# Kernel optimization log

Measured on AMD Instinct MI355X. Metric: run time of the kernel, lower is better.

## Reference

```python
import jax, jax.numpy as jnp
import numpy as np

L, D, C, H = 2, 2, 256, 128  # layers, directions, channels, hidden (= C//2, bidirectional)
B, T = 32, 1024


def setup_inputs() -> dict:
    key = jax.random.key(0)
    ks = jax.random.split(key, 5)
    k = 1.0 / np.sqrt(H)  # PyTorch LSTM init scale
    u = lambda kk, shape: jax.random.uniform(kk, shape, jnp.float32, -k, k)
    return {
        "x": jax.random.normal(ks[0], (B, C, T), jnp.float32),
        "W_ih": u(ks[1], (L, D, 4 * H, C)),  # layer1 input is concat(fwd,bwd) = C wide too
        "W_hh": u(ks[2], (L, D, 4 * H, H)),
        "b_ih": u(ks[3], (L, D, 4 * H)),
        "b_hh": u(ks[4], (L, D, 4 * H)),
    }


def _lstm_dir(xs, Wih, Whh, bih, bhh, reverse):
    # xs: [T, B, C_in] time-major; returns hidden states [T, B, H]
    Tn, Bn, _ = xs.shape
    Hh = Whh.shape[1]
    # precompute input contribution to all gates for every timestep (one big GEMM)
    gx = jnp.einsum('tbc,gc->tbg', xs, Wih) + bih + bhh  # [T, B, 4H]

    def step(carry, g):
        h, c = carry
        g = g + h @ Whh.T  # [B, 4H]
        i, f, gg, o = jnp.split(g, 4, axis=-1)  # PyTorch gate order: i, f, g, o
        c = jax.nn.sigmoid(f) * c + jax.nn.sigmoid(i) * jnp.tanh(gg)
        h = jax.nn.sigmoid(o) * jnp.tanh(c)
        return (h, c), h

    init = (jnp.zeros((Bn, Hh), xs.dtype), jnp.zeros((Bn, Hh), xs.dtype))
    _, hs = jax.lax.scan(step, init, gx, reverse=reverse)
    return hs


def reference(x, W_ih, W_hh, b_ih, b_hh):
    # x: [B, C, T] -> time-major [T, B, C] (matches x.transpose(1,2) with batch_first)
    h = jnp.transpose(x, (2, 0, 1))
    for l in range(L):
        fwd = _lstm_dir(h, W_ih[l, 0], W_hh[l, 0], b_ih[l, 0], b_hh[l, 0], False)
        bwd = _lstm_dir(h, W_ih[l, 1], W_hh[l, 1], b_ih[l, 1], b_hh[l, 1], True)
        h = jnp.concatenate([fwd, bwd], axis=-1)  # [T, B, 2H] = [T, B, C]
    # back to [B, C, T] (matches out.transpose(1,2))
    return jnp.transpose(h, (1, 2, 0))
```

## Files before the change

kernel.cpp:

```cpp
#include <hip/hip_runtime.h>
#include <cstdint>
#include <cstddef>

static constexpr int TT = 1024;
static constexpr int BB = 32;
static constexpr int CC = 256;
static constexpr int HH = 128;
static constexpr int GG = 512;
static constexpr int MM = TT * BB;

typedef float f32x2 __attribute__((ext_vector_type(2)));
typedef float f32x4v __attribute__((ext_vector_type(4)));
typedef short bf16x8 __attribute__((ext_vector_type(8)));

__device__ __forceinline__ float fsig(float x) { return 1.f / (1.f + __expf(-x)); }
__device__ __forceinline__ float ftanh(float x) {
  float e = __expf(2.f * x);
  return 1.f - 2.f / (e + 1.f);
}
__device__ __forceinline__ ushort bf16_rn(float x) {
  union { float f; uint u; } v; v.f = x;
  const uint r = v.u + 0x7fffu + ((v.u >> 16) & 1u);
  return (ushort)(r >> 16);
}
__device__ __forceinline__ float bf16_to_f(ushort h) {
  union { uint u; float f; } v; v.u = ((uint)h) << 16;
  return v.f;
}
__device__ __forceinline__ uint pack2(ushort a, ushort b) { return (uint)a | ((uint)b << 16); }

__global__ __launch_bounds__(256) void k_transpose_cvt_in(const float* __restrict__ x,
                                                          ushort* __restrict__ xhi,
                                                          ushort* __restrict__ xlo) {
  __shared__ float tile[32][33];
  const int t0 = blockIdx.x * 32, c0 = blockIdx.y * 32, b = blockIdx.z;
  const int tx = threadIdx.x, ty = threadIdx.y;
#pragma unroll
  for (int i = 0; i < 4; i++) {
    const int cc = ty + i * 8;
    tile[cc][tx] = x[((size_t)b * CC + (c0 + cc)) * TT + t0 + tx];
  }
  __syncthreads();
#pragma unroll
  for (int i = 0; i < 4; i++) {
    const int tt = ty + i * 8;
    const float v = tile[tx][tt];
    const ushort hi = bf16_rn(v);
    const size_t idx = ((size_t)(t0 + tt) * BB + b) * CC + c0 + tx;
    xhi[idx] = hi;
    xlo[idx] = bf16_rn(v - bf16_to_f(hi));
  }
}

__global__ __launch_bounds__(256) void k_transpose_out(const float* __restrict__ h2,
                                                       float* __restrict__ out) {
  __shared__ float tile[32][33];
  const int t0 = blockIdx.x * 32, c0 = blockIdx.y * 32, b = blockIdx.z;
  const int tx = threadIdx.x, ty = threadIdx.y;
#pragma unroll
  for (int i = 0; i < 4; i++) {
    const int tt = ty + i * 8;
    tile[tt][tx] = h2[((size_t)(t0 + tt) * BB + b) * CC + c0 + tx];
  }
  __syncthreads();
#pragma unroll
  for (int i = 0; i < 4; i++) {
    const int cc = ty + i * 8;
    out[((size_t)b * CC + (c0 + cc)) * TT + t0 + tx] = tile[tx][cc];
  }
}

__global__ __launch_bounds__(256) void k_gemm_mfma(const ushort* __restrict__ Ahi,
                                                   const ushort* __restrict__ Alo,
                                                   const float* __restrict__ W,
                                                   const float* __restrict__ bih,
                                                   const float* __restrict__ bhh,
                                                   float* __restrict__ gx) {
  const int d = blockIdx.z;
  const int g0 = blockIdx.x * 64;
  const int m0 = blockIdx.y * 128;
  const float* Wd = W + (size_t)d * GG * CC;

  __shared__ ushort Ah[128][64];
  __shared__ ushort Al[128][64];
  __shared__ ushort Bh[64][64];
  __shared__ ushort Bl[64][64];

  const int tid = threadIdx.x;
  const int lane = tid & 63;
  const int wid = tid >> 6;
  const int wm = (wid >> 1) * 64;
  const int wg = (wid & 1) * 32;

  f32x4v acc[4][2] = {};

  for (int k0 = 0; k0 < CC; k0 += 64) {
    __syncthreads();
#pragma unroll
    for (int c = 0; c < 4; c++) {
      const int f8 = c * 256 + tid;
      const int r = f8 >> 3;
      const int kb = f8 & 7;
      const int sw = (kb ^ (r & 7)) << 3;
      const uint4 vh = *(const uint4*)&Ahi[(size_t)(m0 + r) * CC + k0 + kb * 8];
      const uint4 vl = *(const uint4*)&Alo[(size_t)(m0 + r) * CC + k0 + kb * 8];
      *(uint4*)&Ah[r][sw] = vh;
      *(uint4*)&Al[r][sw] = vl;
    }
#pragma unroll
    for (int c = 0; c < 4; c++) {
      const int f4 = c * 256 + tid;
      const int g = f4 >> 4;
      const int k4 = f4 & 15;
      const float4 wv = *(const float4*)&Wd[(size_t)(g0 + g) * CC + k0 + k4 * 4];
      ushort h0 = bf16_rn(wv.x), h1 = bf16_rn(wv.y), h2 = bf16_rn(wv.z), h3 = bf16_rn(wv.w);
      ushort l0 = bf16_rn(wv.x - bf16_to_f(h0)), l1 = bf16_rn(wv.y - bf16_to_f(h1));
      ushort l2 = bf16_rn(wv.z - bf16_to_f(h2)), l3 = bf16_rn(wv.w - bf16_to_f(h3));
      const int off = (((k4 >> 1) ^ (g & 7)) << 3) | ((k4 & 1) * 4);
      uint2 ph; ph.x = pack2(h0, h1); ph.y = pack2(h2, h3);
      uint2 pl; pl.x = pack2(l0, l1); pl.y = pack2(l2, l3);
      *(uint2*)&Bh[g][off] = ph;
      *(uint2*)&Bl[g][off] = pl;
    }
    __syncthreads();
#pragma unroll
    for (int h = 0; h < 2; h++) {
      const int kb = h * 4 + (lane >> 4);
      bf16x8 afh[4], afl[4], bfh[2], bfl[2];
#pragma unroll
      for (int i = 0; i < 4; i++) {
        const int row = wm + i * 16 + (lane & 15);
        const int sw = (kb ^ (row & 7)) << 3;
        afh[i] = *(const bf16x8*)&Ah[row][sw];
        afl[i] = *(const bf16x8*)&Al[row][sw];
      }
#pragma unroll
      for (int j = 0; j < 2; j++) {
        const int gr = wg + j * 16 + (lane & 15);
        const int sw = (kb ^ (gr & 7)) << 3;
        bfh[j] = *(const bf16x8*)&Bh[gr][sw];
        bfl[j] = *(const bf16x8*)&Bl[gr][sw];
      }
#pragma unroll
      for (int i = 0; i < 4; i++)
#pragma unroll
        for (int j = 0; j < 2; j++) {
          acc[i][j] = __builtin_amdgcn_mfma_f32_16x16x32_bf16(afh[i], bfh[j], acc[i][j], 0, 0, 0);
          acc[i][j] = __builtin_amdgcn_mfma_f32_16x16x32_bf16(afh[i], bfl[j], acc[i][j], 0, 0, 0);
          acc[i][j] = __builtin_amdgcn_mfma_f32_16x16x32_bf16(afl[i], bfh[j], acc[i][j], 0, 0, 0);
        }
    }
  }
  const int col = lane & 15;
  const int rbase = (lane >> 4) * 4;
#pragma unroll
  for (int j = 0; j < 2; j++) {
    const int g = g0 + wg + j * 16 + col;
    const float bias = bih[d * GG + g] + bhh[d * GG + g];
#pragma unroll
    for (int i = 0; i < 4; i++) {
      const int mrow = m0 + wm + i * 16 + rbase;
#pragma unroll
      for (int rr = 0; rr < 4; rr++)
        gx[((size_t)d * MM + mrow + rr) * GG + g] = acc[i][j][rr] + bias;
    }
  }
}

__global__ __launch_bounds__(512, 1) void k_lstm_rec(const float* __restrict__ gx,
                                                     const float* __restrict__ Whh,
                                                     float* __restrict__ hf32,
                                                     ushort* __restrict__ hhi,
                                                     ushort* __restrict__ hlo,
                                                     int store_bf16) {
  const int b = blockIdx.x & 31;
  const int d = blockIdx.x >> 5;
  const int tid = threadIdx.x;
  const int q = tid >> 7;
  const int j = tid & 127;
  __shared__ __align__(16) float h_s[HH];
  __shared__ __align__(16) float part[4][HH][4];

  f32x2 w2[4][16];
  {
    const float* base = Whh + (size_t)d * GG * HH;
#pragma unroll
    for (int gi = 0; gi < 4; gi++) {
      const float4* wrow = (const float4*)(base + (size_t)(gi * HH + j) * HH + q * 32);
#pragma unroll
      for (int k = 0; k < 8; k++) {
        const float4 t4 = wrow[k];
        w2[gi][2 * k] = f32x2{t4.x, t4.y};
        w2[gi][2 * k + 1] = f32x2{t4.z, t4.w};
      }
    }
  }
#pragma unroll
  for (int gi = 0; gi < 4; gi++)
#pragma unroll
    for (int k = 0; k < 16; k++)
      asm volatile("" : "+v"(w2[gi][k]));

  if (tid < HH) h_s[tid] = 0.f;
  float c = 0.f;

  const float* gxb = gx + ((size_t)d * TT * BB + b) * (size_t)GG;
  const size_t stride = (size_t)BB * GG;
  int t = d ? (TT - 1) : 0;
  const int tdir = d ? -1 : 1;
  const bool is_act = (tid < HH);

  float gxc0 = 0.f, gxc1 = 0.f, gxc2 = 0.f, gxc3 = 0.f;
  if (is_act) {
    const float* g0 = gxb + (size_t)t * stride + j;
    gxc0 = g0[0]; gxc1 = g0[HH]; gxc2 = g0[2 * HH]; gxc3 = g0[3 * HH];
  }
  __syncthreads();

  for (int s = 0; s < TT; s++) {
    float gxn0 = 0.f, gxn1 = 0.f, gxn2 = 0.f, gxn3 = 0.f;
    if (is_act && s + 1 < TT) {
      const float* g0 = gxb + (size_t)(t + tdir) * stride + j;
      gxn0 = g0[0]; gxn1 = g0[HH]; gxn2 = g0[2 * HH]; gxn3 = g0[3 * HH];
    }

    f32x2 hp[16];
    {
      const float4* hq = (const float4*)(h_s + q * 32);
#pragma unroll
      for (int k = 0; k < 8; k++) {
        const float4 hv = hq[k];
        hp[2 * k] = f32x2{hv.x, hv.y};
        hp[2 * k + 1] = f32x2{hv.z, hv.w};
      }
    }

    f32x2 aA0 = {0.f, 0.f}, aA1 = {0.f, 0.f}, aA2 = {0.f, 0.f}, aA3 = {0.f, 0.f};
    f32x2 aB0 = {0.f, 0.f}, aB1 = {0.f, 0.f}, aB2 = {0.f, 0.f}, aB3 = {0.f, 0.f};
#pragma unroll
    for (int k = 0; k < 8; k++) {
      aA0 = w2[0][2 * k] * hp[2 * k] + aA0;  aB0 = w2[0][2 * k + 1] * hp[2 * k + 1] + aB0;
      aA1 = w2[1][2 * k] * hp[2 * k] + aA1;  aB1 = w2[1][2 * k + 1] * hp[2 * k + 1] + aB1;
      aA2 = w2[2][2 * k] * hp[2 * k] + aA2;  aB2 = w2[2][2 * k + 1] * hp[2 * k + 1] + aB2;
      aA3 = w2[3][2 * k] * hp[2 * k] + aA3;  aB3 = w2[3][2 * k + 1] * hp[2 * k + 1] + aB3;
    }
    const float A0 = (aA0.x + aA0.y) + (aB0.x + aB0.y);
    const float A1 = (aA1.x + aA1.y) + (aB1.x + aB1.y);
    const float A2 = (aA2.x + aA2.y) + (aB2.x + aB2.y);
    const float A3 = (aA3.x + aA3.y) + (aB3.x + aB3.y);
    *(float4*)&part[q][j][0] = make_float4(A0, A1, A2, A3);
    __syncthreads();

    if (is_act) {
      const float4 p0 = *(const float4*)&part[0][j][0];
      const float4 p1 = *(const float4*)&part[1][j][0];
      const float4 p2 = *(const float4*)&part[2][j][0];
      const float4 p3 = *(const float4*)&part[3][j][0];
      const float i_g = fsig(p0.x + p1.x + p2.x + p3.x + gxc0);
      const float f_g = fsig(p0.y + p1.y + p2.y + p3.y + gxc1);
      const float g_g = ftanh(p0.z + p1.z + p2.z + p3.z + gxc2);
      const float o_g = fsig(p0.w + p1.w + p2.w + p3.w + gxc3);
      c = f_g * c + i_g * g_g;
      const float h = o_g * ftanh(c);
      h_s[j] = h;
      const size_t idx = ((size_t)t * BB + b) * CC + d * HH + j;
      if (store_bf16) {
        const ushort hi = bf16_rn(h);
        hhi[idx] = hi;
        hlo[idx] = bf16_rn(h - bf16_to_f(hi));
      } else {
        hf32[idx] = h;
      }
    }
    __syncthreads();
    gxc0 = gxn0; gxc1 = gxn1; gxc2 = gxn2; gxc3 = gxn3;
    t += tdir;
  }
}

extern "C" void kernel_launch(void* const* d_in, const int* in_sizes, int n_in,
                              void* d_out, int out_size, void* d_ws, size_t ws_size,
                              hipStream_t stream) {
  const float* x    = (const float*)d_in[0];
  const float* W_ih = (const float*)d_in[1];
  const float* W_hh = (const float*)d_in[2];
  const float* b_ih = (const float*)d_in[3];
  const float* b_hh = (const float*)d_in[4];
  float* out = (float*)d_out;

  if (ws_size < (size_t)160 * 1024 * 1024) return;

  char* ws = (char*)d_ws;
  ushort* abf_hi = (ushort*)ws;
  ushort* abf_lo = (ushort*)(ws + (size_t)16 * 1024 * 1024);
  float*  h2     = (float*)ws;
  float*  gxbuf  = (float*)(ws + (size_t)32 * 1024 * 1024);

  const dim3 tb(32, 8);
  const dim3 tg(TT / 32, CC / 32, BB);
  const dim3 gemm_grid(GG / 64, MM / 128, 2);

  k_transpose_cvt_in<<<tg, tb, 0, stream>>>(x, abf_hi, abf_lo);
  k_gemm_mfma<<<gemm_grid, 256, 0, stream>>>(abf_hi, abf_lo, W_ih, b_ih, b_hh, gxbuf);
  k_lstm_rec<<<64, 512, 0, stream>>>(gxbuf, W_hh, nullptr, abf_hi, abf_lo, 1);
  k_gemm_mfma<<<gemm_grid, 256, 0, stream>>>(abf_hi, abf_lo, W_ih + 2 * GG * CC,
                                             b_ih + 2 * GG, b_hh + 2 * GG, gxbuf);
  k_lstm_rec<<<64, 512, 0, stream>>>(gxbuf, W_hh + 2 * GG * HH, h2, nullptr, nullptr, 0);
  k_transpose_out<<<tg, tb, 0, stream>>>(h2, out);
}
```

Before: 1.819 ms.

## Reduce LSTM recurrence partials via lane shuffles and double-buffer hidden state

The recurrent kernel now places the four K-quarter partial sums of each hidden unit in adjacent lanes of one wavefront and combines them with xor-shuffles, replacing the shared-memory partial array and one of the two block barriers per timestep. The hidden state is double-buffered in LDS so a single barrier per step suffices. That barrier waits only on LDS counters, not on global stores. Every thread now runs the gate math redundantly, and the h outputs are written by different lanes to spread the stores. The intent is to cut per-step synchronisation latency on the serial time loop.

```diff
diff --git a/kernel.cpp b/kernel.cpp
--- a/kernel.cpp
+++ b/kernel.cpp
@@ -9,7 +9,6 @@
 static constexpr int GG = 512;
 static constexpr int MM = TT * BB;
 
-typedef float f32x2 __attribute__((ext_vector_type(2)));
 typedef float f32x4v __attribute__((ext_vector_type(4)));
 typedef short bf16x8 __attribute__((ext_vector_type(8)));
 
@@ -28,6 +27,12 @@
   return v.f;
 }
 __device__ __forceinline__ uint pack2(ushort a, ushort b) { return (uint)a | ((uint)b << 16); }
+
+__device__ __forceinline__ void barrier_lds_only() {
+  asm volatile("s_waitcnt lgkmcnt(0)" ::: "memory");
+  __builtin_amdgcn_s_barrier();
+  asm volatile("" ::: "memory");
+}
 
 __global__ __launch_bounds__(256) void k_transpose_cvt_in(const float* __restrict__ x,
                                                           ushort* __restrict__ xhi,
@@ -176,103 +181,92 @@
   const int b = blockIdx.x & 31;
   const int d = blockIdx.x >> 5;
   const int tid = threadIdx.x;
-  const int q = tid >> 7;
-  const int j = tid & 127;
-  __shared__ __align__(16) float h_s[HH];
-  __shared__ __align__(16) float part[4][HH][4];
-
-  f32x2 w2[4][16];
+  const int lane = tid & 63;
+  const int m = lane >> 2;
+  const int q = lane & 3;
+  const int j = (tid >> 6) * 16 + m;
+
+  __shared__ __align__(16) float h_s[2][HH];
+
+  float4 w4[4][8];
   {
     const float* base = Whh + (size_t)d * GG * HH;
 #pragma unroll
     for (int gi = 0; gi < 4; gi++) {
       const float4* wrow = (const float4*)(base + (size_t)(gi * HH + j) * HH + q * 32);
 #pragma unroll
-      for (int k = 0; k < 8; k++) {
-        const float4 t4 = wrow[k];
-        w2[gi][2 * k] = f32x2{t4.x, t4.y};
-        w2[gi][2 * k + 1] = f32x2{t4.z, t4.w};
-      }
+      for (int k = 0; k < 8; k++) w4[gi][k] = wrow[k];
     }
   }
 #pragma unroll
   for (int gi = 0; gi < 4; gi++)
 #pragma unroll
-    for (int k = 0; k < 16; k++)
-      asm volatile("" : "+v"(w2[gi][k]));
-
-  if (tid < HH) h_s[tid] = 0.f;
+    for (int k = 0; k < 8; k++)
+      asm volatile("" : "+v"(w4[gi][k].x), "+v"(w4[gi][k].y), "+v"(w4[gi][k].z), "+v"(w4[gi][k].w));
+
+  if (tid < HH) h_s[0][tid] = 0.f;
   float c = 0.f;
 
   const float* gxb = gx + ((size_t)d * TT * BB + b) * (size_t)GG;
   const size_t stride = (size_t)BB * GG;
   int t = d ? (TT - 1) : 0;
   const int tdir = d ? -1 : 1;
-  const bool is_act = (tid < HH);
-
-  float gxc0 = 0.f, gxc1 = 0.f, gxc2 = 0.f, gxc3 = 0.f;
-  if (is_act) {
+
+  float gxc0, gxc1, gxc2, gxc3;
+  {
     const float* g0 = gxb + (size_t)t * stride + j;
     gxc0 = g0[0]; gxc1 = g0[HH]; gxc2 = g0[2 * HH]; gxc3 = g0[3 * HH];
   }
   __syncthreads();
 
+  int p = 0;
   for (int s = 0; s < TT; s++) {
     float gxn0 = 0.f, gxn1 = 0.f, gxn2 = 0.f, gxn3 = 0.f;
-    if (is_act && s + 1 < TT) {
+    if (s + 1 < TT) {
       const float* g0 = gxb + (size_t)(t + tdir) * stride + j;
       gxn0 = g0[0]; gxn1 = g0[HH]; gxn2 = g0[2 * HH]; gxn3 = g0[3 * HH];
     }
 
-    f32x2 hp[16];
-    {
-      const float4* hq = (const float4*)(h_s + q * 32);
-#pragma unroll
-      for (int k = 0; k < 8; k++) {
-        const float4 hv = hq[k];
-        hp[2 * k] = f32x2{hv.x, hv.y};
-        hp[2 * k + 1] = f32x2{hv.z, hv.w};
+    const float4* hq = (const float4*)&h_s[p][q * 32];
+    float a0 = 0.f, a1 = 0.f, a2 = 0.f, a3 = 0.f;
+#pragma unroll
+    for (int k = 0; k < 8; k++) {
+      const float4 hv = hq[k];
+      a0 = fmaf(w4[0][k].x, hv.x, a0); a0 = fmaf(w4[0][k].y, hv.y, a0);
+      a0 = fmaf(w4[0][k].z, hv.z, a0); a0 = fmaf(w4[0][k].w, hv.w, a0);
+      a1 = fmaf(w4[1][k].x, hv.x, a1); a1 = fmaf(w4[1][k].y, hv.y, a1);
+      a1 = fmaf(w4[1][k].z, hv.z, a1); a1 = fmaf(w4[1][k].w, hv.w, a1);
+      a2 = fmaf(w4[2][k].x, hv.x, a2); a2 = fmaf(w4[2][k].y, hv.y, a2);
+      a2 = fmaf(w4[2][k].z, hv.z, a2); a2 = fmaf(w4[2][k].w, hv.w, a2);
+      a3 = fmaf(w4[3][k].x, hv.x, a3); a3 = fmaf(w4[3][k].y, hv.y, a3);
+      a3 = fmaf(w4[3][k].z, hv.z, a3); a3 = fmaf(w4[3][k].w, hv.w, a3);
+    }
+    a0 += __shfl_xor(a0, 1, 64); a0 += __shfl_xor(a0, 2, 64);
+    a1 += __shfl_xor(a1, 1, 64); a1 += __shfl_xor(a1, 2, 64);
+    a2 += __shfl_xor(a2, 1, 64); a2 += __shfl_xor(a2, 2, 64);
+    a3 += __shfl_xor(a3, 1, 64); a3 += __shfl_xor(a3, 2, 64);
+
+    const float i_g = fsig(a0 + gxc0);
+    const float f_g = fsig(a1 + gxc1);
+    const float g_g = ftanh(a2 + gxc2);
+    const float o_g = fsig(a3 + gxc3);
+    c = f_g * c + i_g * g_g;
+    const float h = o_g * ftanh(c);
+
+    const size_t idx = ((size_t)t * BB + b) * CC + d * HH + j;
+    if (q == 0) h_s[p ^ 1][j] = h;
+    if (store_bf16) {
+      if (q == 2) hhi[idx] = bf16_rn(h);
+      if (q == 3) {
+        const ushort hi = bf16_rn(h);
+        hlo[idx] = bf16_rn(h - bf16_to_f(hi));
       }
-    }
-
-    f32x2 aA0 = {0.f, 0.f}, aA1 = {0.f, 0.f}, aA2 = {0.f, 0.f}, aA3 = {0.f, 0.f};
-    f32x2 aB0 = {0.f, 0.f}, aB1 = {0.f, 0.f}, aB2 = {0.f, 0.f}, aB3 = {0.f, 0.f};
-#pragma unroll
-    for (int k = 0; k < 8; k++) {
-      aA0 = w2[0][2 * k] * hp[2 * k] + aA0;  aB0 = w2[0][2 * k + 1] * hp[2 * k + 1] + aB0;
-      aA1 = w2[1][2 * k] * hp[2 * k] + aA1;  aB1 = w2[1][2 * k + 1] * hp[2 * k + 1] + aB1;
-      aA2 = w2[2][2 * k] * hp[2 * k] + aA2;  aB2 = w2[2][2 * k + 1] * hp[2 * k + 1] + aB2;
-      aA3 = w2[3][2 * k] * hp[2 * k] + aA3;  aB3 = w2[3][2 * k + 1] * hp[2 * k + 1] + aB3;
-    }
-    const float A0 = (aA0.x + aA0.y) + (aB0.x + aB0.y);
-    const float A1 = (aA1.x + aA1.y) + (aB1.x + aB1.y);
-    const float A2 = (aA2.x + aA2.y) + (aB2.x + aB2.y);
-    const float A3 = (aA3.x + aA3.y) + (aB3.x + aB3.y);
-    *(float4*)&part[q][j][0] = make_float4(A0, A1, A2, A3);
-    __syncthreads();
-
-    if (is_act) {
-      const float4 p0 = *(const float4*)&part[0][j][0];
-      const float4 p1 = *(const float4*)&part[1][j][0];
-      const float4 p2 = *(const float4*)&part[2][j][0];
-      const float4 p3 = *(const float4*)&part[3][j][0];
-      const float i_g = fsig(p0.x + p1.x + p2.x + p3.x + gxc0);
-      const float f_g = fsig(p0.y + p1.y + p2.y + p3.y + gxc1);
-      const float g_g = ftanh(p0.z + p1.z + p2.z + p3.z + gxc2);
-      const float o_g = fsig(p0.w + p1.w + p2.w + p3.w + gxc3);
-      c = f_g * c + i_g * g_g;
-      const float h = o_g * ftanh(c);
-      h_s[j] = h;
-      const size_t idx = ((size_t)t * BB + b) * CC + d * HH + j;
-      if (store_bf16) {
-        const ushort hi = bf16_rn(h);
-        hhi[idx] = hi;
-        hlo[idx] = bf16_rn(h - bf16_to_f(hi));
-      } else {
-        hf32[idx] = h;
-      }
-    }
-    __syncthreads();
+    } else {
+      if (q == 1) hf32[idx] = h;
+    }
+
+    barrier_lds_only();
+    p ^= 1;
     gxc0 = gxn0; gxc1 = gxn1; gxc2 = gxn2; gxc3 = gxn3;
     t += tdir;
   }
```

Result: slower. 2.314 ms (+27.3%).
